# Kernel tuning notes

Measured on AMD Instinct MI355X. Metric: run time of the kernel, lower is better.

The kernel has to match this reference:

```python
import jax, jax.numpy as jnp
import numpy as np

TAU = 2.0
SUR_ALPHA = 4.0  # spikingjelly surrogate.Sigmoid default alpha
LN_EPS = 1e-5
SCALE = 0.125
NUM_HEADS = 16


@jax.custom_vjp
def _spike(u):
    return (u >= 0.0).astype(u.dtype)

def _spike_fwd(u):
    return _spike(u), u

def _spike_bwd(u, g):
    s = jax.nn.sigmoid(SUR_ALPHA * u)
    return (g * SUR_ALPHA * s * (1.0 - s),)

_spike.defvjp(_spike_fwd, _spike_bwd)


def lif(x, v_th=1.0):
    # Single-step LIF from fresh state v=0, v_reset=0:
    # v_post = v + (x - v)/tau = x/tau; spike = H(v_post - v_th)
    return _spike(x / TAU - v_th)


def ln(x, g, b):
    m = jnp.mean(x, axis=-1, keepdims=True)
    v = jnp.var(x, axis=-1, keepdims=True)
    return (x - m) * jax.lax.rsqrt(v + LN_EPS) * g + b


def setup_inputs() -> dict:
    key = jax.random.key(0)
    ks = jax.random.split(key, 8)
    B, L, D = 4, 1024, 1024
    HID = 4096
    s_d = 1.0 / np.sqrt(D)
    s_h = 1.0 / np.sqrt(HID)
    return {
        "x": jax.random.normal(ks[0], (B, L, D), jnp.float32),
        "q_w": jax.random.normal(ks[1], (D, D), jnp.float32) * s_d,
        "q_g": jnp.ones((D,), jnp.float32),
        "q_b": jnp.zeros((D,), jnp.float32),
        "k_w": jax.random.normal(ks[2], (D, D), jnp.float32) * s_d,
        "k_g": jnp.ones((D,), jnp.float32),
        "k_b": jnp.zeros((D,), jnp.float32),
        "v_w": jax.random.normal(ks[3], (D, D), jnp.float32) * s_d,
        "v_g": jnp.ones((D,), jnp.float32),
        "v_b": jnp.zeros((D,), jnp.float32),
        "proj_w": jax.random.normal(ks[4], (D, D), jnp.float32) * s_d,
        "proj_bias": jnp.zeros((D,), jnp.float32),
        "proj_g": jnp.ones((D,), jnp.float32),
        "proj_beta": jnp.zeros((D,), jnp.float32),
        "fc1_w": jax.random.normal(ks[5], (D, HID), jnp.float32) * s_d,
        "fc1_bias": jnp.zeros((HID,), jnp.float32),
        "fc1_g": jnp.ones((HID,), jnp.float32),
        "fc1_beta": jnp.zeros((HID,), jnp.float32),
        "fc2_w": jax.random.normal(ks[6], (HID, D), jnp.float32) * s_h,
        "fc2_bias": jnp.zeros((D,), jnp.float32),
        "fc2_g": jnp.ones((D,), jnp.float32),
        "fc2_beta": jnp.zeros((D,), jnp.float32),
    }


def reference(x, q_w, q_g, q_b, k_w, k_g, k_b, v_w, v_g, v_b,
              proj_w, proj_bias, proj_g, proj_beta,
              fc1_w, fc1_bias, fc1_g, fc1_beta,
              fc2_w, fc2_bias, fc2_g, fc2_beta):
    B, L, D = x.shape
    H = NUM_HEADS
    hd = D // H

    # --- SSA ---
    q = lif(ln(x @ q_w, q_g, q_b))  # (B,L,D), binary spikes
    k = lif(ln(x @ k_w, k_g, k_b))
    v = lif(ln(x @ v_w, v_g, v_b))
    q = q.reshape(B, L, H, hd).transpose(0, 2, 1, 3)  # (B,H,L,hd)
    k = k.reshape(B, L, H, hd).transpose(0, 2, 1, 3)
    v = v.reshape(B, L, H, hd).transpose(0, 2, 1, 3)

    attn = jnp.einsum('bhqd,bhkd->bhqk', q, k) * SCALE  # no softmax
    y = jnp.einsum('bhqk,bhkd->bhqd', attn, v)
    y = y.transpose(0, 2, 1, 3).reshape(B, L, D)
    y = lif(y, v_th=0.5)                    # attn_lif (v_threshold=0.5)
    y = lif(ln(y @ proj_w + proj_bias, proj_g, proj_beta))

    x = x + y  # residual 1

    # --- MLP ---
    m = lif(ln(x @ fc1_w + fc1_bias, fc1_g, fc1_beta))
    m = lif(ln(m @ fc2_w + fc2_bias, fc2_g, fc2_beta))

    return x + m  # residual 2
```

## Files before the change

### kernel.cpp

```cpp
#include <hip/hip_runtime.h>
#include <hip/hip_bf16.h>


#define NB 4
#define LL 1024
#define DIM 1024
#define NH 16
#define HDIM 64
#define HID 4096
#define NROWS (NB * LL)

typedef unsigned short u16;
typedef __attribute__((ext_vector_type(8))) short short8v;
typedef __attribute__((ext_vector_type(4))) float f32x4;

__device__ __forceinline__ u16 f2bf(float f) {
    unsigned u = __builtin_bit_cast(unsigned, f);
    return (u16)((u + 0x7fffu + ((u >> 16) & 1u)) >> 16);
}
__device__ __forceinline__ float bf2f(u16 h) {
    unsigned u = ((unsigned)h) << 16;
    return __builtin_bit_cast(float, u);
}
__device__ __forceinline__ void split3v(float v, u16& a, u16& b, u16& c) {
    a = f2bf(v);
    float r = v - bf2f(a);
    b = f2bf(r);
    float r2 = r - bf2f(b);
    c = f2bf(r2);
}

__global__ __launch_bounds__(256) void split3_rows(
    const float* __restrict__ X, u16* __restrict__ Xs, int K)
{
    const int row = blockIdx.y;
    const int c4 = (blockIdx.x * 256 + threadIdx.x) * 4;
    if (c4 >= K) return;
    float4 v = *(const float4*)(X + (size_t)row * K + c4);
    float vv[4] = {v.x, v.y, v.z, v.w};
    u16 h0[4], h1[4], h2[4];
#pragma unroll
    for (int j = 0; j < 4; ++j) split3v(vv[j], h0[j], h1[j], h2[j]);
    u16* base = Xs + (size_t)row * 3 * K + c4;
    *(uint2*)(base + 0 * K) = *(uint2*)h0;
    *(uint2*)(base + 1 * K) = *(uint2*)h1;
    *(uint2*)(base + 2 * K) = *(uint2*)h2;
}

__global__ __launch_bounds__(256) void split_wt(
    const float* __restrict__ W, u16* __restrict__ Wt, int K, int N, int ldwt)
{
    __shared__ float tile[64][65];
    const int k0 = blockIdx.y * 64, n0 = blockIdx.x * 64;
    const int t = threadIdx.x;
    const int rr = t >> 4;
    const int cc = (t & 15) * 4;
#pragma unroll
    for (int it = 0; it < 4; ++it) {
        const int k = rr + it * 16;
        float4 v = *(const float4*)(W + (size_t)(k0 + k) * N + n0 + cc);
        tile[cc + 0][k] = v.x; tile[cc + 1][k] = v.y;
        tile[cc + 2][k] = v.z; tile[cc + 3][k] = v.w;
    }
    __syncthreads();
    const int n = t >> 2, kc = (t & 3) * 16;
    u16 h0[16], h1[16], h2[16];
#pragma unroll
    for (int j = 0; j < 16; ++j)
        split3v(tile[n][kc + j], h0[j], h1[j], h2[j]);
    u16* base = Wt + (size_t)(n0 + n) * ldwt + k0 + kc;
    *(uint4*)(base + 0 * K)     = ((uint4*)h0)[0];
    *(uint4*)(base + 0 * K + 8) = ((uint4*)h0)[1];
    *(uint4*)(base + 1 * K)     = ((uint4*)h1)[0];
    *(uint4*)(base + 1 * K + 8) = ((uint4*)h1)[1];
    *(uint4*)(base + 2 * K)     = ((uint4*)h2)[0];
    *(uint4*)(base + 2 * K + 8) = ((uint4*)h2)[1];
}

#define AS1G const __attribute__((address_space(1))) void*
#define AS3L __attribute__((address_space(3))) void*

__global__ __launch_bounds__(512, 2) void gemm256(
    const u16* __restrict__ A, int lda,
    const u16* __restrict__ Bt, int ldb,
    unsigned apack, unsigned bpack, int nt,
    const float* __restrict__ bias,
    float* __restrict__ Out, int ldo)
{
    __shared__ u16 As2[2][16384];
    __shared__ u16 Bs2[2][16384];
    const int t = threadIdx.x;
    const int wid = t >> 6, lane = t & 63;
    const int wm = wid >> 2, wn = wid & 3;
    int bid = blockIdx.y * gridDim.x + blockIdx.x;
    const int nwg = gridDim.x * gridDim.y;
    bid = (bid & 7) * (nwg >> 3) + (bid >> 3);
    const int row0 = (bid / gridDim.x) * 256, col0 = (bid % gridDim.x) * 256;
    const int lrow = lane & 15, lk = lane >> 4;
    const int sr0 = t >> 3;
    const int scol = ((t & 7) ^ (sr0 & 7)) * 8;

    f32x4 acc[8][4];
#pragma unroll
    for (int i = 0; i < 8; ++i)
#pragma unroll
        for (int j = 0; j < 4; ++j) acc[i][j] = f32x4{0.f, 0.f, 0.f, 0.f};
    short8v afA[4][2], afB[4][2], bf[2][2];

#define STA(bs, Rb, c0)                                                        \
    __builtin_amdgcn_global_load_lds(                                          \
        (AS1G)(A + (size_t)(row0 + (Rb) + sr0) * lda + (c0) + scol),           \
        (AS3L)(&As2[bs][(Rb) * 64 + t * 8]), 16, 0, 0);
#define STB(bs, Rb, c0)                                                        \
    {                                                                          \
        const int _rho = (Rb) + sr0;                                           \
        const int _bc = ((_rho >> 5) & 3) * 64 + ((_rho >> 7) << 5) + (_rho & 31); \
        __builtin_amdgcn_global_load_lds(                                      \
            (AS1G)(Bt + (size_t)(col0 + _bc) * ldb + (c0) + scol),             \
            (AS3L)(&Bs2[bs][(Rb) * 64 + t * 8]), 16, 0, 0);                    \
    }
#define STPAIR0(bs, cA, cB) STA(bs, 0, cA)   STA(bs, 128, cA)
#define STPAIR1(bs, cA, cB) STB(bs, 0, cB)   STB(bs, 64, cB)
#define STPAIR2(bs, cA, cB) STA(bs, 64, cA)  STA(bs, 192, cA)
#define STPAIR3(bs, cA, cB) STB(bs, 128, cB) STB(bs, 192, cB)

#define VMW(n) asm volatile("s_waitcnt vmcnt(" #n ")" ::: "memory");
#define BAR  __builtin_amdgcn_s_barrier();
#define BARP                                                                   \
    __builtin_amdgcn_s_barrier();                                              \
    __builtin_amdgcn_sched_barrier(0);

#define LDA(dst, MQ, P)                                                        \
    _Pragma("unroll")                                                          \
    for (int mf = 0; mf < 4; ++mf) {                                           \
        const int r = wm * 128 + (MQ) * 64 + mf * 16 + lrow;                   \
        _Pragma("unroll")                                                      \
        for (int ks = 0; ks < 2; ++ks) {                                       \
            const int slot = (lk + ks * 4) ^ (r & 7);                          \
            dst[mf][ks] = *(const short8v*)&As2[P][r * 64 + slot * 8];         \
        }                                                                      \
    }
#define LDB(NQ, P)                                                             \
    _Pragma("unroll")                                                          \
    for (int nf = 0; nf < 2; ++nf) {                                           \
        const int rho = (NQ) * 128 + (wn >> 1) * 64 + (wn & 1) * 32            \
                        + nf * 16 + lrow;                                      \
        _Pragma("unroll")                                                      \
        for (int ks = 0; ks < 2; ++ks) {                                       \
            const int slot = (lk + ks * 4) ^ (rho & 7);                        \
            bf[nf][ks] = *(const short8v*)&Bs2[P][rho * 64 + slot * 8];        \
        }                                                                      \
    }
#define MM(asrc, MQ, NQ)                                                       \
    __builtin_amdgcn_s_setprio(1);                                             \
    _Pragma("unroll")                                                          \
    for (int mf = 0; mf < 4; ++mf)                                             \
        _Pragma("unroll")                                                      \
        for (int nf = 0; nf < 2; ++nf)                                         \
            _Pragma("unroll")                                                  \
            for (int ks = 0; ks < 2; ++ks)                                     \
                acc[(MQ) * 4 + mf][(NQ) * 2 + nf] =                            \
                    __builtin_amdgcn_mfma_f32_16x16x32_bf16(                   \
                        asrc[mf][ks], bf[nf][ks],                              \
                        acc[(MQ) * 4 + mf][(NQ) * 2 + nf], 0, 0, 0);           \
    __builtin_amdgcn_s_setprio(0);

    {
        const int cA = (apack & 15) * 1024;
        const int cB = (bpack & 15) * 1024;
        STPAIR0(0, cA, cB) STPAIR1(0, cA, cB)
        STPAIR2(0, cA, cB) STPAIR3(0, cA, cB)
    }

    for (int kt = 0; kt < nt - 1; ++kt) {
        const int p = kt & 1, np = p ^ 1;
        const int nkt = kt + 1;
        const int nns = nkt >> 4, nk0 = (nkt & 15) * 64;
        const int nA = (int)((apack >> (nns * 4)) & 15) * 1024 + nk0;
        const int nB = (int)((bpack >> (nns * 4)) & 15) * 1024 + nk0;
        VMW(4) BARP
        LDA(afA, 0, p) LDB(0, p) STPAIR0(np, nA, nB) MM(afA, 0, 0)
        VMW(4) BAR
        LDA(afB, 1, p) STPAIR1(np, nA, nB) MM(afB, 1, 0)
        VMW(4) BAR
        LDB(1, p) STPAIR2(np, nA, nB) MM(afB, 1, 1)
        BAR
        STPAIR3(np, nA, nB) MM(afA, 0, 1)
    }
    {
        const int p = (nt - 1) & 1;
        VMW(4) BARP LDA(afA, 0, p) LDB(0, p) MM(afA, 0, 0)
        VMW(2) BAR  LDA(afB, 1, p) MM(afB, 1, 0)
        VMW(0) BAR  LDB(1, p) MM(afB, 1, 1)
        BAR         MM(afA, 0, 1)
    }
#undef STPAIR0
#undef STPAIR1
#undef STPAIR2
#undef STPAIR3
#undef LDA
#undef LDB
#undef MM

#pragma unroll
    for (int ni = 0; ni < 4; ++ni) {
        const int col = col0 + wn * 64 + ni * 16 + lrow;
        const float bv = bias ? bias[col] : 0.f;
#pragma unroll
        for (int mi = 0; mi < 8; ++mi) {
            const int rbase = row0 + wm * 128 + mi * 16 + lk * 4;
#pragma unroll
            for (int r = 0; r < 4; ++r)
                Out[(size_t)(rbase + r) * ldo + col] = acc[mi][ni][r] + bv;
        }
    }
#undef STA
#undef STB
#undef VMW
#undef BAR
#undef BARP
}

struct SegList { int a[6]; int b[6]; int n; };

template <int BN_>
__global__ __launch_bounds__(256) void gemm_mfma(
    const u16* __restrict__ A, int lda,
    const u16* __restrict__ Bt, int ldb,
    SegList segs, int Kseg,
    const float* __restrict__ bias,
    float* __restrict__ Out, int ldo)
{
    constexpr int NF = BN_ / 32;
    __shared__ u16 As[128 * 64];
    __shared__ u16 Bs[BN_ * 64];
    const int t = threadIdx.x;
    const int wid = t >> 6, lane = t & 63;
    const int wr = wid >> 1, wc = wid & 1;
    const int z = blockIdx.z;
    const int koff = z * Kseg;
    Out += (size_t)z * (size_t)gridDim.y * 128 * ldo;
    int bid = blockIdx.y * gridDim.x + blockIdx.x;
    const int nwg = gridDim.x * gridDim.y;
    bid = (bid & 7) * (nwg >> 3) + (bid >> 3);
    const int row0 = (bid / gridDim.x) * 128, col0 = (bid % gridDim.x) * BN_;
    const int lrow = lane & 15;
    const int s_subrow = lane >> 3;
    const int s_slot   = (lane & 7) ^ (lane >> 3);
    const int s_coff   = s_slot * 8;

    f32x4 acc[4][NF];
#pragma unroll
    for (int i = 0; i < 4; ++i)
#pragma unroll
        for (int j = 0; j < NF; ++j) acc[i][j] = f32x4{0.f, 0.f, 0.f, 0.f};

    for (int s = 0; s < segs.n; ++s) {
        const u16* pa = A + segs.a[s] + koff;
        const u16* pb = Bt + segs.b[s] + koff;
        for (int k0 = 0; k0 < Kseg; k0 += 64) {
            asm volatile("s_waitcnt lgkmcnt(0)" ::: "memory");
            __syncthreads();
#pragma unroll
            for (int c = 0; c < 4; ++c) {
                const int chunk = wid * 4 + c;
                const int rg = row0 + chunk * 8 + s_subrow;
                __builtin_amdgcn_global_load_lds(
                    (AS1G)(pa + (size_t)rg * lda + k0 + s_coff),
                    (AS3L)(&As[chunk * 512 + lane * 8]), 16, 0, 0);
            }
#pragma unroll
            for (int c = 0; c < NF; ++c) {
                const int chunk = wid * NF + c;
                const int rg = col0 + chunk * 8 + s_subrow;
                __builtin_amdgcn_global_load_lds(
                    (AS1G)(pb + (size_t)rg * ldb + k0 + s_coff),
                    (AS3L)(&Bs[chunk * 512 + lane * 8]), 16, 0, 0);
            }
            asm volatile("s_waitcnt vmcnt(0)" ::: "memory");
            __syncthreads();
#pragma unroll
            for (int ksub = 0; ksub < 2; ++ksub) {
                short8v af[4], bfr[NF];
#pragma unroll
                for (int f = 0; f < 4; ++f) {
                    const int ra = wr * 64 + f * 16 + lrow;
                    const int slot = ((lane >> 4) + ksub * 4) ^ (lrow & 7);
                    af[f] = *(const short8v*)&As[ra * 64 + slot * 8];
                }
#pragma unroll
                for (int f = 0; f < NF; ++f) {
                    const int rb = wc * (BN_ / 2) + f * 16 + lrow;
                    const int slot = ((lane >> 4) + ksub * 4) ^ (lrow & 7);
                    bfr[f] = *(const short8v*)&Bs[rb * 64 + slot * 8];
                }
#pragma unroll
                for (int i = 0; i < 4; ++i)
#pragma unroll
                    for (int j = 0; j < NF; ++j)
                        acc[i][j] = __builtin_amdgcn_mfma_f32_16x16x32_bf16(
                            af[i], bfr[j], acc[i][j], 0, 0, 0);
            }
        }
    }
#pragma unroll
    for (int j = 0; j < NF; ++j) {
        const int col = col0 + wc * (BN_ / 2) + j * 16 + lrow;
        const float bv = (bias && z == 0) ? bias[col] : 0.f;
#pragma unroll
        for (int i = 0; i < 4; ++i) {
            const int rbase = row0 + wr * 64 + i * 16 + (lane >> 4) * 4;
#pragma unroll
            for (int r = 0; r < 4; ++r)
                Out[(size_t)(rbase + r) * ldo + col] = acc[i][j][r] + bv;
        }
    }
}

template <int DN>
__global__ __launch_bounds__(256) void lnlif2(
    const float* __restrict__ U, const float* __restrict__ U2, int ld, int coloff,
    const float* __restrict__ g, const float* __restrict__ beta,
    const float* __restrict__ resid,
    u16* __restrict__ spike_bf16,
    float* __restrict__ out_f32,
    u16* __restrict__ split3_out)
{
    constexpr int PT = DN / 1024;
    const int r = blockIdx.x, t = threadIdx.x;
    const float4* u4 = (const float4*)(U + (size_t)r * ld + coloff);
    const float4* u24 = U2 ? (const float4*)(U2 + (size_t)r * ld + coloff) : nullptr;
    float4 vals[PT];
    float lsum = 0.f;
#pragma unroll
    for (int i = 0; i < PT; ++i) {
        vals[i] = u4[t + i * 256];
        if (u24) {
            float4 w = u24[t + i * 256];
            vals[i].x += w.x; vals[i].y += w.y;
            vals[i].z += w.z; vals[i].w += w.w;
        }
        lsum += (vals[i].x + vals[i].y) + (vals[i].z + vals[i].w);
    }
    __shared__ float red[4];
    __shared__ float bcast;
    for (int o = 32; o > 0; o >>= 1) lsum += __shfl_down(lsum, o);
    if ((t & 63) == 0) red[t >> 6] = lsum;
    __syncthreads();
    if (t == 0) bcast = (red[0] + red[1] + red[2] + red[3]) * (1.f / DN);
    __syncthreads();
    const float m = bcast;
    float lss = 0.f;
#pragma unroll
    for (int i = 0; i < PT; ++i) {
        float dx = vals[i].x - m, dy = vals[i].y - m;
        float dz = vals[i].z - m, dw = vals[i].w - m;
        lss += (dx * dx + dy * dy) + (dz * dz + dw * dw);
    }
    for (int o = 32; o > 0; o >>= 1) lss += __shfl_down(lss, o);
    if ((t & 63) == 0) red[t >> 6] = lss;
    __syncthreads();
    if (t == 0) bcast = (red[0] + red[1] + red[2] + red[3]) * (1.f / DN);
    __syncthreads();
    const float rs = 1.f / sqrtf(bcast + 1e-5f);
#pragma unroll
    for (int i = 0; i < PT; ++i) {
        const int c = (t + i * 256) * 4;
        const size_t idx = (size_t)r * DN + c;
        const float4 gg = *(const float4*)(g + c);
        const float4 bb = *(const float4*)(beta + c);
        float sv[4];
        sv[0] = ((vals[i].x - m) * rs * gg.x + bb.x >= 2.0f) ? 1.f : 0.f;
        sv[1] = ((vals[i].y - m) * rs * gg.y + bb.y >= 2.0f) ? 1.f : 0.f;
        sv[2] = ((vals[i].z - m) * rs * gg.z + bb.z >= 2.0f) ? 1.f : 0.f;
        sv[3] = ((vals[i].w - m) * rs * gg.w + bb.w >= 2.0f) ? 1.f : 0.f;
        if (spike_bf16) {
            u16 sp[4];
#pragma unroll
            for (int j = 0; j < 4; ++j) sp[j] = sv[j] != 0.f ? (u16)0x3F80 : (u16)0;
            *(uint2*)(spike_bf16 + idx) = *(uint2*)sp;
        }
        if (out_f32 || split3_out) {
            float4 rv = resid ? *(const float4*)(resid + idx)
                              : float4{0.f, 0.f, 0.f, 0.f};
            float vv[4] = {rv.x + sv[0], rv.y + sv[1], rv.z + sv[2], rv.w + sv[3]};
            if (out_f32) {
                float4 ov = {vv[0], vv[1], vv[2], vv[3]};
                *(float4*)(out_f32 + idx) = ov;
            }
            if (split3_out) {
                u16 h0[4], h1[4], h2[4];
#pragma unroll
                for (int j = 0; j < 4; ++j) split3v(vv[j], h0[j], h1[j], h2[j]);
                u16* base = split3_out + (size_t)r * 3 * DN + c;
                *(uint2*)(base + 0 * DN) = *(uint2*)h0;
                *(uint2*)(base + 1 * DN) = *(uint2*)h1;
                *(uint2*)(base + 2 * DN) = *(uint2*)h2;
            }
        }
    }
}

__global__ __launch_bounds__(256) void ktv_part(
    const u16* __restrict__ Sk, const u16* __restrict__ Sv,
    float* __restrict__ ktvp)
{
    const int bh = blockIdx.x, ck = blockIdx.y;
    const int b = bh >> 4, h = bh & 15;
    __shared__ float kch[64][64];
    __shared__ float vch[64][64];
    const int t = threadIdx.x;
    const int i = t >> 2;
    const int j0 = (t & 3) << 4;
    float4 a0 = {0,0,0,0}, a1 = {0,0,0,0}, a2 = {0,0,0,0}, a3 = {0,0,0,0};
    for (int l0 = ck * 256; l0 < ck * 256 + 256; l0 += 64) {
        __syncthreads();
#pragma unroll
        for (int q = 0; q < 2; ++q) {
            const int chunk = t + q * 256;
            const int li = chunk >> 3, c8 = (chunk & 7) << 3;
            const size_t off = ((size_t)b * LL + l0 + li) * DIM + h * HDIM + c8;
            union { uint4 v; u16 s[8]; } uk, uv;
            uk.v = *(const uint4*)(Sk + off);
            uv.v = *(const uint4*)(Sv + off);
#pragma unroll
            for (int j = 0; j < 8; ++j) {
                kch[li][c8 + j] = uk.s[j] ? 1.f : 0.f;
                vch[li][c8 + j] = uv.s[j] ? 1.f : 0.f;
            }
        }
        __syncthreads();
        for (int l = 0; l < 64; ++l) {
            if (kch[l][i] != 0.f) {
                const float4 v0 = *(float4*)&vch[l][j0];
                const float4 v1 = *(float4*)&vch[l][j0 + 4];
                const float4 v2 = *(float4*)&vch[l][j0 + 8];
                const float4 v3 = *(float4*)&vch[l][j0 + 12];
                a0.x += v0.x; a0.y += v0.y; a0.z += v0.z; a0.w += v0.w;
                a1.x += v1.x; a1.y += v1.y; a1.z += v1.z; a1.w += v1.w;
                a2.x += v2.x; a2.y += v2.y; a2.z += v2.z; a2.w += v2.w;
                a3.x += v3.x; a3.y += v3.y; a3.z += v3.z; a3.w += v3.w;
            }
        }
    }
    const size_t o = (((size_t)ck * 64 + bh) * 64 + i) * 64 + j0;
    *(float4*)(ktvp + o)      = a0;
    *(float4*)(ktvp + o + 4)  = a1;
    *(float4*)(ktvp + o + 8)  = a2;
    *(float4*)(ktvp + o + 12) = a3;
}

__global__ __launch_bounds__(256) void qktv_bf16(
    const u16* __restrict__ Sq, const float* __restrict__ ktvp,
    u16* __restrict__ Y)
{
    const int bh = blockIdx.x, ck = blockIdx.y;
    const int b = bh >> 4, h = bh & 15;
    __shared__ float kt[64][64];
    const int t = threadIdx.x;
#pragma unroll
    for (int q = 0; q < 16; ++q) {
        const int idx = t + q * 256;
        ((float*)kt)[idx] = (ktvp[((size_t)0 * 64 + bh) * 4096 + idx]
                           + ktvp[((size_t)1 * 64 + bh) * 4096 + idx])
                          + (ktvp[((size_t)2 * 64 + bh) * 4096 + idx]
                           + ktvp[((size_t)3 * 64 + bh) * 4096 + idx]);
    }
    __syncthreads();
    const int li = t >> 6;
    const int j = t & 63;
    for (int l0 = ck * 128; l0 < ck * 128 + 128; l0 += 4) {
        const size_t roff = ((size_t)b * LL + l0 + li) * DIM + h * HDIM;
        const u16 sqv = Sq[roff + j];
        unsigned long long mask = __ballot(sqv != 0);
        float acc = 0.f;
        while (mask) {
            const int i = __ffsll((unsigned long long)mask) - 1;
            mask &= mask - 1;
            acc += kt[i][j];
        }
        const float y = 0.125f * acc;
        Y[roff + j] = (y >= 1.0f) ? (u16)0x3F80 : (u16)0;
    }
}

#define BM 128
#define BN 128
#define BK 16

__global__ __launch_bounds__(256) void gemm_f32(
    const float* __restrict__ A, const float* __restrict__ W,
    const float* __restrict__ bias, float* __restrict__ U,
    int M, int K, int N)
{
    __shared__ float As[BK][BM];
    __shared__ float Bs[BK][BN];
    const int t = threadIdx.x;
    const int tx = t & 15, ty = t >> 4;
    const int row0 = blockIdx.y * BM, col0 = blockIdx.x * BN;
    const int ar = t >> 2;
    const int ac = (t & 3) << 2;
    const int br = t >> 5;
    const int bc = (t & 31) << 2;
    float acc[8][8];
#pragma unroll
    for (int i = 0; i < 8; ++i)
#pragma unroll
        for (int j = 0; j < 8; ++j) acc[i][j] = 0.f;
    for (int k0 = 0; k0 < K; k0 += BK) {
        float4 va0 = *(const float4*)(A + (size_t)(row0 + ar) * K + k0 + ac);
        float4 va1 = *(const float4*)(A + (size_t)(row0 + ar + 64) * K + k0 + ac);
        float4 vb0 = *(const float4*)(W + (size_t)(k0 + br) * N + col0 + bc);
        float4 vb1 = *(const float4*)(W + (size_t)(k0 + br + 8) * N + col0 + bc);
        __syncthreads();
        As[ac + 0][ar] = va0.x; As[ac + 1][ar] = va0.y;
        As[ac + 2][ar] = va0.z; As[ac + 3][ar] = va0.w;
        As[ac + 0][ar + 64] = va1.x; As[ac + 1][ar + 64] = va1.y;
        As[ac + 2][ar + 64] = va1.z; As[ac + 3][ar + 64] = va1.w;
        *(float4*)&Bs[br][bc] = vb0;
        *(float4*)&Bs[br + 8][bc] = vb1;
        __syncthreads();
#pragma unroll
        for (int kk = 0; kk < BK; ++kk) {
            float4 fa0 = *(float4*)&As[kk][ty * 8];
            float4 fa1 = *(float4*)&As[kk][ty * 8 + 4];
            float4 fb0 = *(float4*)&Bs[kk][tx * 8];
            float4 fb1 = *(float4*)&Bs[kk][tx * 8 + 4];
            float av[8] = {fa0.x, fa0.y, fa0.z, fa0.w, fa1.x, fa1.y, fa1.z, fa1.w};
            float bv[8] = {fb0.x, fb0.y, fb0.z, fb0.w, fb1.x, fb1.y, fb1.z, fb1.w};
#pragma unroll
            for (int i = 0; i < 8; ++i)
#pragma unroll
                for (int j = 0; j < 8; ++j)
                    acc[i][j] += av[i] * bv[j];
        }
    }
    float bvals[8];
#pragma unroll
    for (int j = 0; j < 8; ++j)
        bvals[j] = bias ? bias[col0 + tx * 8 + j] : 0.f;
#pragma unroll
    for (int i = 0; i < 8; ++i) {
        const int row = row0 + ty * 8 + i;
        float* dst = U + (size_t)row * N + col0 + tx * 8;
        float4 o0, o1;
        o0.x = acc[i][0] + bvals[0]; o0.y = acc[i][1] + bvals[1];
        o0.z = acc[i][2] + bvals[2]; o0.w = acc[i][3] + bvals[3];
        o1.x = acc[i][4] + bvals[4]; o1.y = acc[i][5] + bvals[5];
        o1.z = acc[i][6] + bvals[6]; o1.w = acc[i][7] + bvals[7];
        *(float4*)dst = o0;
        *(float4*)(dst + 4) = o1;
    }
}

template <int DN>
__global__ __launch_bounds__(256) void lnlif_old(
    const float* __restrict__ U, const float* __restrict__ g,
    const float* __restrict__ beta, float thr,
    const float* __restrict__ resid, float* __restrict__ out)
{
    constexpr int PT = DN / 256;
    const int r = blockIdx.x, t = threadIdx.x;
    const float* u = U + (size_t)r * DN;
    float vals[PT];
    float lsum = 0.f;
#pragma unroll
    for (int i = 0; i < PT; ++i) { vals[i] = u[t + i * 256]; lsum += vals[i]; }
    __shared__ float red[4];
    __shared__ float bc0;
    for (int o = 32; o > 0; o >>= 1) lsum += __shfl_down(lsum, o);
    if ((t & 63) == 0) red[t >> 6] = lsum;
    __syncthreads();
    if (t == 0) bc0 = (red[0] + red[1] + red[2] + red[3]) * (1.f / DN);
    __syncthreads();
    const float m = bc0;
    float lss = 0.f;
#pragma unroll
    for (int i = 0; i < PT; ++i) { float d = vals[i] - m; lss += d * d; }
    for (int o = 32; o > 0; o >>= 1) lss += __shfl_down(lss, o);
    if ((t & 63) == 0) red[t >> 6] = lss;
    __syncthreads();
    if (t == 0) bc0 = (red[0] + red[1] + red[2] + red[3]) * (1.f / DN);
    __syncthreads();
    const float rs = 1.0f / sqrtf(bc0 + 1e-5f);
#pragma unroll
    for (int i = 0; i < PT; ++i) {
        const int c = t + i * 256;
        const float nrm = (vals[i] - m) * rs * g[c] + beta[c];
        const float s = (nrm >= thr) ? 1.0f : 0.0f;
        out[(size_t)r * DN + c] = resid ? (resid[(size_t)r * DN + c] + s) : s;
    }
}

__global__ __launch_bounds__(256) void ktv_f32(
    const float* __restrict__ Sk, const float* __restrict__ Sv,
    float* __restrict__ ktvb)
{
    const int bh = blockIdx.x;
    const int b = bh >> 4, h = bh & 15;
    __shared__ float kch[64][64];
    __shared__ float vch[64][64];
    const int t = threadIdx.x;
    const int i = t >> 2;
    const int j0 = (t & 3) << 4;
    float4 a0 = {0,0,0,0}, a1 = {0,0,0,0}, a2 = {0,0,0,0}, a3 = {0,0,0,0};
    for (int l0 = 0; l0 < LL; l0 += 64) {
        __syncthreads();
#pragma unroll
        for (int q = 0; q < 4; ++q) {
            const int idx = t + q * 256;
            const int li = idx >> 4, c4 = (idx & 15) << 2;
            const size_t off = ((size_t)b * LL + l0 + li) * DIM + h * HDIM + c4;
            *(float4*)&kch[li][c4] = *(const float4*)(Sk + off);
            *(float4*)&vch[li][c4] = *(const float4*)(Sv + off);
        }
        __syncthreads();
        for (int l = 0; l < 64; ++l) {
            if (kch[l][i] != 0.f) {
                const float4 v0 = *(float4*)&vch[l][j0];
                const float4 v1 = *(float4*)&vch[l][j0 + 4];
                const float4 v2 = *(float4*)&vch[l][j0 + 8];
                const float4 v3 = *(float4*)&vch[l][j0 + 12];
                a0.x += v0.x; a0.y += v0.y; a0.z += v0.z; a0.w += v0.w;
                a1.x += v1.x; a1.y += v1.y; a1.z += v1.z; a1.w += v1.w;
                a2.x += v2.x; a2.y += v2.y; a2.z += v2.z; a2.w += v2.w;
                a3.x += v3.x; a3.y += v3.y; a3.z += v3.z; a3.w += v3.w;
            }
        }
    }
    const size_t o = ((size_t)bh * 64 + i) * 64 + j0;
    *(float4*)(ktvb + o)      = a0;
    *(float4*)(ktvb + o + 4)  = a1;
    *(float4*)(ktvb + o + 8)  = a2;
    *(float4*)(ktvb + o + 12) = a3;
}

__global__ __launch_bounds__(256) void qktv_f32(
    const float* __restrict__ Sq, const float* __restrict__ ktvb,
    float* __restrict__ Y)
{
    const int bh = blockIdx.x;
    const int b = bh >> 4, h = bh & 15;
    __shared__ float kt[64][64];
    const int t = threadIdx.x;
#pragma unroll
    for (int q = 0; q < 16; ++q) {
        const int idx = t + q * 256;
        ((float*)kt)[idx] = ktvb[(size_t)bh * 4096 + idx];
    }
    __syncthreads();
    const int li = t >> 6;
    const int j = t & 63;
    for (int l0 = 0; l0 < LL; l0 += 4) {
        const size_t roff = ((size_t)b * LL + l0 + li) * DIM + h * HDIM;
        const float sqv = Sq[roff + j];
        unsigned long long mask = __ballot(sqv != 0.f);
        float acc = 0.f;
        while (mask) {
            const int i = __ffsll((unsigned long long)mask) - 1;
            mask &= mask - 1;
            acc += kt[i][j];
        }
        const float y = 0.125f * acc;
        Y[roff + j] = (y >= 1.0f) ? 1.0f : 0.0f;
    }
}

extern "C" void kernel_launch(void* const* d_in, const int* in_sizes, int n_in,
                              void* d_out, int out_size, void* d_ws, size_t ws_size,
                              hipStream_t stream)
{
    const float* x        = (const float*)d_in[0];
    const float* q_w      = (const float*)d_in[1];
    const float* q_g      = (const float*)d_in[2];
    const float* q_b      = (const float*)d_in[3];
    const float* k_w      = (const float*)d_in[4];
    const float* k_g      = (const float*)d_in[5];
    const float* k_b      = (const float*)d_in[6];
    const float* v_w      = (const float*)d_in[7];
    const float* v_g      = (const float*)d_in[8];
    const float* v_b      = (const float*)d_in[9];
    const float* proj_w   = (const float*)d_in[10];
    const float* proj_bias= (const float*)d_in[11];
    const float* proj_g   = (const float*)d_in[12];
    const float* proj_beta= (const float*)d_in[13];
    const float* fc1_w    = (const float*)d_in[14];
    const float* fc1_bias = (const float*)d_in[15];
    const float* fc1_g    = (const float*)d_in[16];
    const float* fc1_beta = (const float*)d_in[17];
    const float* fc2_w    = (const float*)d_in[18];
    const float* fc2_bias = (const float*)d_in[19];
    const float* fc2_g    = (const float*)d_in[20];
    const float* fc2_beta = (const float*)d_in[21];

    const dim3 blk(256);
    const size_t NEEDED = 143654912;

    if (ws_size >= NEEDED) {
        char* ws = (char*)d_ws;
        float* U    = (float*)ws;
        float* Up2  = U + (size_t)NROWS * DIM;
        u16*   Xsh  = (u16*)(ws + 67108864);
        u16*   Wbuf = (u16*)(ws + 100663296);
        u16*   Sq   = (u16*)(ws + 125829120);
        u16*   Sk   = (u16*)(ws + 134217728);
        u16*   SvYb = (u16*)((char*)Xsh + 25165824);
        u16*   Xs   = Xsh;
        u16*   X1s  = Xsh;
        u16*   Sm   = Xsh;
        float* X1   = (float*)d_out;
        float* ktvp = (float*)(ws + 100663296);

        const int pa6[6] = {0, 1, 2, 0, 1, 0}, pb6[6] = {0, 1, 0, 2, 0, 1};
        unsigned apack = 0, bpack = 0;
        for (int i = 0; i < 6; ++i) {
            apack |= (unsigned)pa6[i] << (4 * i);
            bpack |= (unsigned)pb6[i] << (4 * i);
        }
        SegList segP;
        {
            for (int i = 0; i < 6; ++i) { segP.a[i] = 0; segP.b[i] = 0; }
            segP.b[1] = 1024; segP.b[2] = 2048; segP.n = 3;
        }
        SegList segF2;
        {
            for (int i = 0; i < 6; ++i) { segF2.a[i] = 0; segF2.b[i] = 0; }
            segF2.b[1] = 4096; segF2.b[2] = 8192; segF2.n = 3;
        }

        split3_rows<<<dim3(1, NROWS), blk, 0, stream>>>(x, Xs, DIM);

        split_wt<<<dim3(16, 16), blk, 0, stream>>>(q_w, Wbuf,               DIM, DIM, 3072);
        split_wt<<<dim3(16, 16), blk, 0, stream>>>(k_w, Wbuf + 1024 * 3072, DIM, DIM, 3072);
        split_wt<<<dim3(16, 16), blk, 0, stream>>>(v_w, Wbuf + 2048 * 3072, DIM, DIM, 3072);
        gemm256<<<dim3(12, 16), dim3(512), 0, stream>>>(
            Xs, 3072, Wbuf, 3072, apack, bpack, 96, nullptr, U, 3072);
        lnlif2<DIM><<<NROWS, blk, 0, stream>>>(U, nullptr, 3072, 0,    q_g, q_b, nullptr, Sq,   nullptr, nullptr);
        lnlif2<DIM><<<NROWS, blk, 0, stream>>>(U, nullptr, 3072, 1024, k_g, k_b, nullptr, Sk,   nullptr, nullptr);
        lnlif2<DIM><<<NROWS, blk, 0, stream>>>(U, nullptr, 3072, 2048, v_g, v_b, nullptr, SvYb, nullptr, nullptr);

        ktv_part<<<dim3(NB * NH, 4), blk, 0, stream>>>(Sk, SvYb, ktvp);
        qktv_bf16<<<dim3(NB * NH, 8), blk, 0, stream>>>(Sq, ktvp, SvYb);

        split_wt<<<dim3(16, 16), blk, 0, stream>>>(proj_w, Wbuf, DIM, DIM, 3072);
        gemm_mfma<64><<<dim3(16, 32, 2), blk, 0, stream>>>(
            SvYb, 1024, Wbuf, 3072, segP, 512, proj_bias, U, DIM);
        lnlif2<DIM><<<NROWS, blk, 0, stream>>>(U, Up2, DIM, 0, proj_g, proj_beta, x, nullptr, X1, X1s);

        split_wt<<<dim3(64, 16), blk, 0, stream>>>(fc1_w, Wbuf, DIM, HID, 3072);
        gemm256<<<dim3(16, 16), dim3(512), 0, stream>>>(
            X1s, 3072, Wbuf, 3072, apack, bpack, 96, fc1_bias, U, HID);
        lnlif2<HID><<<NROWS, blk, 0, stream>>>(U, nullptr, HID, 0, fc1_g, fc1_beta, nullptr, Sm, nullptr, nullptr);

        split_wt<<<dim3(16, 64), blk, 0, stream>>>(fc2_w, Wbuf, HID, DIM, 12288);
        gemm_mfma<64><<<dim3(16, 32, 2), blk, 0, stream>>>(
            Sm, 4096, Wbuf, 12288, segF2, 2048, fc2_bias, U, DIM);
        lnlif2<DIM><<<NROWS, blk, 0, stream>>>(U, Up2, DIM, 0, fc2_g, fc2_beta, X1, nullptr, (float*)d_out, nullptr);
        return;
    }

    float* U    = (float*)d_ws;
    float* Sq   = U + (size_t)1 * NROWS * DIM;
    float* Sk   = U + (size_t)2 * NROWS * DIM;
    float* Sv   = U + (size_t)3 * NROWS * DIM;
    float* Yb   = Sv;
    float* ktvb = U + (size_t)NROWS * HID;
    float* Y2   = ktvb + (size_t)NB * NH * HDIM * HDIM;
    float* X1   = (float*)d_out;
    float* outf = (float*)d_out;

    const dim3 gemm_d(DIM / BN, NROWS / BM);
    const dim3 gemm_h(HID / BN, NROWS / BM);

    gemm_f32<<<gemm_d, blk, 0, stream>>>(x, q_w, nullptr, U, NROWS, DIM, DIM);
    lnlif_old<DIM><<<NROWS, blk, 0, stream>>>(U, q_g, q_b, 2.0f, nullptr, Sq);
    gemm_f32<<<gemm_d, blk, 0, stream>>>(x, k_w, nullptr, U, NROWS, DIM, DIM);
    lnlif_old<DIM><<<NROWS, blk, 0, stream>>>(U, k_g, k_b, 2.0f, nullptr, Sk);
    gemm_f32<<<gemm_d, blk, 0, stream>>>(x, v_w, nullptr, U, NROWS, DIM, DIM);
    lnlif_old<DIM><<<NROWS, blk, 0, stream>>>(U, v_g, v_b, 2.0f, nullptr, Sv);

    ktv_f32<<<NB * NH, blk, 0, stream>>>(Sk, Sv, ktvb);
    qktv_f32<<<NB * NH, blk, 0, stream>>>(Sq, ktvb, Yb);

    gemm_f32<<<gemm_d, blk, 0, stream>>>(Yb, proj_w, proj_bias, U, NROWS, DIM, DIM);
    lnlif_old<DIM><<<NROWS, blk, 0, stream>>>(U, proj_g, proj_beta, 2.0f, x, X1);

    gemm_f32<<<gemm_h, blk, 0, stream>>>(X1, fc1_w, fc1_bias, U, NROWS, DIM, HID);
    lnlif_old<HID><<<NROWS, blk, 0, stream>>>(U, fc1_g, fc1_beta, 2.0f, nullptr, U);

    gemm_f32<<<gemm_d, blk, 0, stream>>>(U, fc2_w, fc2_bias, Y2, NROWS, HID, DIM);
    lnlif_old<DIM><<<NROWS, blk, 0, stream>>>(Y2, fc2_g, fc2_beta, 2.0f, X1, outf);
}
```

Before: 588.8 us.

## Deepen GEMM global-to-LDS prefetch to two tiles ahead

Restructures the double-buffered GEMM main loop so global-to-LDS loads for tile k+2 are issued while tile k is computed, instead of prefetching only the next tile. The prologue now stages two tiles, and the A and B halves of the refill are grouped into whole-tile stages. They are issued once each buffer region has been read into registers. Partial vmcnt waits (10, 8) let some loads for the current tile stay in flight. This aims to hide more global memory latency behind MFMA work. The cost is tighter waitcnt and barrier ordering that must stay correct.

```diff
diff --git a/kernel.cpp b/kernel.cpp
--- a/kernel.cpp
+++ b/kernel.cpp
@@ -119,10 +119,8 @@
             (AS1G)(Bt + (size_t)(col0 + _bc) * ldb + (c0) + scol),             \
             (AS3L)(&Bs2[bs][(Rb) * 64 + t * 8]), 16, 0, 0);                    \
     }
-#define STPAIR0(bs, cA, cB) STA(bs, 0, cA)   STA(bs, 128, cA)
-#define STPAIR1(bs, cA, cB) STB(bs, 0, cB)   STB(bs, 64, cB)
-#define STPAIR2(bs, cA, cB) STA(bs, 64, cA)  STA(bs, 192, cA)
-#define STPAIR3(bs, cA, cB) STB(bs, 128, cB) STB(bs, 192, cB)
+#define STAGE_A(bs, cA) STA(bs, 0, cA) STA(bs, 128, cA) STA(bs, 64, cA) STA(bs, 192, cA)
+#define STAGE_B(bs, cB) STB(bs, 0, cB) STB(bs, 64, cB) STB(bs, 128, cB) STB(bs, 192, cB)
 
 #define VMW(n) asm volatile("s_waitcnt vmcnt(" #n ")" ::: "memory");
 #define BAR  __builtin_amdgcn_s_barrier();
@@ -166,38 +164,45 @@
     __builtin_amdgcn_s_setprio(0);
 
     {
-        const int cA = (apack & 15) * 1024;
-        const int cB = (bpack & 15) * 1024;
-        STPAIR0(0, cA, cB) STPAIR1(0, cA, cB)
-        STPAIR2(0, cA, cB) STPAIR3(0, cA, cB)
+        const int cA0 = (apack & 15) * 1024;
+        const int cB0 = (bpack & 15) * 1024;
+        STAGE_A(0, cA0) STAGE_B(0, cB0)
+        const int cA1 = (apack & 15) * 1024 + 64;
+        const int cB1 = (bpack & 15) * 1024 + 64;
+        STAGE_A(1, cA1) STAGE_B(1, cB1)
     }
 
     for (int kt = 0; kt < nt - 1; ++kt) {
-        const int p = kt & 1, np = p ^ 1;
-        const int nkt = kt + 1;
-        const int nns = nkt >> 4, nk0 = (nkt & 15) * 64;
-        const int nA = (int)((apack >> (nns * 4)) & 15) * 1024 + nk0;
-        const int nB = (int)((bpack >> (nns * 4)) & 15) * 1024 + nk0;
-        VMW(4) BARP
-        LDA(afA, 0, p) LDB(0, p) STPAIR0(np, nA, nB) MM(afA, 0, 0)
-        VMW(4) BAR
-        LDA(afB, 1, p) STPAIR1(np, nA, nB) MM(afB, 1, 0)
-        VMW(4) BAR
-        LDB(1, p) STPAIR2(np, nA, nB) MM(afB, 1, 1)
+        const int p = kt & 1;
+        const int fkt = kt + 2;
+        const bool more2 = fkt < nt;
+        int fA = 0, fB = 0;
+        if (more2) {
+            const int fns = fkt >> 4, fk0 = (fkt & 15) * 64;
+            fA = (int)((apack >> (fns * 4)) & 15) * 1024 + fk0;
+            fB = (int)((bpack >> (fns * 4)) & 15) * 1024 + fk0;
+        }
+        VMW(10) BARP
+        LDA(afA, 0, p) LDB(0, p) MM(afA, 0, 0)
         BAR
-        STPAIR3(np, nA, nB) MM(afA, 0, 1)
+        LDA(afB, 1, p) MM(afB, 1, 0)
+        VMW(8) BAR
+        LDB(1, p)
+        if (more2) { STAGE_A(p, fA) }
+        MM(afB, 1, 1)
+        BAR
+        if (more2) { STAGE_B(p, fB) }
+        MM(afA, 0, 1)
     }
     {
         const int p = (nt - 1) & 1;
-        VMW(4) BARP LDA(afA, 0, p) LDB(0, p) MM(afA, 0, 0)
-        VMW(2) BAR  LDA(afB, 1, p) MM(afB, 1, 0)
+        VMW(2) BARP LDA(afA, 0, p) LDB(0, p) MM(afA, 0, 0)
+        BAR         LDA(afB, 1, p) MM(afB, 1, 0)
         VMW(0) BAR  LDB(1, p) MM(afB, 1, 1)
         BAR         MM(afA, 0, 1)
     }
-#undef STPAIR0
-#undef STPAIR1
-#undef STPAIR2
-#undef STPAIR3
+#undef STAGE_A
+#undef STAGE_B
 #undef LDA
 #undef LDB
 #undef MM
```

Result: slower. 606.4 us (+3.0%).
